# Performance work log

Measured on AMD Instinct MI355X. Metric: run time of the kernel, lower is better.

## Reference

```python
import jax, jax.numpy as jnp
import numpy as np

B = 256          # number of queries
N = 200_000      # active nodes (hidden rows / scatter dim)
E = 400_000      # edges
D = 128          # in_dim == out_dim
ATTN = 128       # attn_dim
N_REL = 24
REL_VOCAB = 2 * N_REL + 3   # 2*n_rel + 1 + 2
N_NODE = 100_000


def setup_inputs() -> dict:
    key = jax.random.key(0)
    ks = jax.random.split(key, 16)
    # forward args
    q_sub = jax.random.randint(ks[0], (B,), 0, N_NODE)
    q_rel = jax.random.randint(ks[1], (B,), 0, REL_VOCAB)
    hidden = jax.random.normal(ks[2], (N, D), dtype=jnp.float32) * 0.05
    # edges columns: [query_idx, unused, rel, tail_entity, sub_local, obj_local]
    e_q = jax.random.randint(ks[3], (E,), 0, B)
    e_unused = jnp.zeros((E,), dtype=jnp.int64)
    e_rel = jax.random.randint(ks[4], (E,), 0, REL_VOCAB)
    e_tail = jax.random.randint(ks[5], (E,), 0, N_NODE)
    e_sub = jax.random.randint(ks[6], (E,), 0, N)
    e_obj = jax.random.randint(ks[7], (E,), 0, N)
    edges = jnp.stack([e_q, e_unused, e_rel, e_tail, e_sub, e_obj], axis=1)
    nodes = jnp.stack([jax.random.randint(ks[8], (N,), 0, B),
                       jax.random.randint(ks[9], (N,), 0, N_NODE)], axis=1)
    # parameters
    rela_embed = jax.random.normal(ks[10], (REL_VOCAB, D), dtype=jnp.float32) * 0.05
    Ws = jax.random.normal(ks[11], (D, ATTN), dtype=jnp.float32) * 0.05
    Wr = jax.random.normal(ks[12], (D, ATTN), dtype=jnp.float32) * 0.05
    Wqr_w = jax.random.normal(ks[13], (D, ATTN), dtype=jnp.float32) * 0.05
    Wqr_b = jnp.zeros((ATTN,), dtype=jnp.float32)
    walpha_w = jax.random.normal(ks[14], (ATTN, 1), dtype=jnp.float32) * 0.05
    walpha_b = jnp.zeros((1,), dtype=jnp.float32)
    Wh = jax.random.normal(ks[15], (D, D), dtype=jnp.float32) * 0.05
    return {"q_sub": q_sub, "q_rel": q_rel, "hidden": hidden, "edges": edges,
            "nodes": nodes, "rela_embed": rela_embed, "Ws": Ws, "Wr": Wr,
            "Wqr_w": Wqr_w, "Wqr_b": Wqr_b, "walpha_w": walpha_w,
            "walpha_b": walpha_b, "Wh": Wh}


def reference(q_sub, q_rel, hidden, edges, nodes, rela_embed, Ws, Wr,
              Wqr_w, Wqr_b, walpha_w, walpha_b, Wh):
    # id_layer == 0 < n_layer-1: no edge filtering branch, act = identity
    sampled_nodes_idx = (nodes[:, 1] > -1) & (nodes[:, 1] < N_NODE + 1)
    sub = edges[:, 4]
    rel = edges[:, 2]
    obj = edges[:, 5]
    r_idx = edges[:, 0]
    hs = hidden[sub]                      # [E, D] gather
    hr = rela_embed[rel]                  # [E, D] gather
    h_qr = rela_embed[q_rel][r_idx]       # [B, D] -> [E, D] gather
    # fused attention MLP: sigmoid(w_alpha(relu(Ws hs + Wr hr + Wqr h_qr + b)))
    pre = jax.nn.relu(hs @ Ws + hr @ Wr + h_qr @ Wqr_w + Wqr_b)   # [E, ATTN]
    alpha = jax.nn.sigmoid(pre @ walpha_w + walpha_b)             # [E, 1]
    message = alpha * (hs + hr)                                   # [E, D]
    message_agg = jax.ops.segment_sum(message, obj, num_segments=N)  # [N, D]
    hidden_new = message_agg @ Wh                                 # [N, D]
    return hidden_new, alpha, sampled_nodes_idx
```

## Files before the change

kernel.cpp:

```cpp
#include <hip/hip_runtime.h>
#include <hip/hip_bf16.h>
#include <math.h>

#define DIM 128
#define N_NODE_C 100000

typedef __attribute__((ext_vector_type(8))) short  bf16x8;
typedef __attribute__((ext_vector_type(4))) float  f32x4;

__device__ inline unsigned short f2bf_rne(float f) {
    unsigned u = __float_as_uint(f);
    return (unsigned short)((u + 0x7FFFu + ((u >> 16) & 1u)) >> 16);
}
__device__ inline float bf2f(unsigned short u) {
    return __uint_as_float(((unsigned)u) << 16);
}

__global__ __launch_bounds__(128) void setup_kernel(
    const int* __restrict__ q_rel,
    const float* __restrict__ rela,
    const float* __restrict__ Wqr_w,
    const float* __restrict__ Wqr_b,
    const float* __restrict__ Wr,
    const float* __restrict__ Ws,
    const float* __restrict__ Wh,
    float* __restrict__ qrW,
    float* __restrict__ relhr,
    uint4* __restrict__ wpack_s,
    uint4* __restrict__ wpack_h,
    int B, int RV)
{
    const int blk = blockIdx.x;
    const int j   = threadIdx.x;

    if (blk < B + RV) {
        __shared__ float emb[DIM];
        const float* W;
        float* out;
        float bias = 0.f;
        int row;
        if (blk < B) {
            row  = q_rel[blk];
            W    = Wqr_w;
            out  = qrW + (size_t)blk * DIM;
            bias = Wqr_b[j];
        } else {
            row = blk - B;
            W   = Wr;
            out = relhr + (size_t)(blk - B) * 256;
        }
        emb[j] = rela[(size_t)row * DIM + j];
        __syncthreads();

        float acc = bias;
#pragma unroll 8
        for (int k = 0; k < DIM; ++k)
            acc += emb[k] * W[k * DIM + j];
        out[j] = acc;
        if (blk >= B)
            out[128 + j] = emb[j];
        return;
    }

    const int pid = blk - (B + RV);
    const float* W = (pid < 16) ? Ws : Wh;
    uint4* dst     = (pid < 16) ? wpack_s : wpack_h;
    const int id   = (pid & 15) * 128 + j;
    const int ct   = id >> 8;
    const int kb   = (id >> 6) & 3;
    const int lane = id & 63;
    const int col  = ct * 16 + (lane & 15);
    const int k0   = kb * 32 + (lane >> 4) * 8;

    unsigned v[4];
#pragma unroll
    for (int p = 0; p < 4; ++p) {
        unsigned lo = f2bf_rne(W[(size_t)(k0 + 2 * p)     * DIM + col]);
        unsigned hi = f2bf_rne(W[(size_t)(k0 + 2 * p + 1) * DIM + col]);
        v[p] = lo | (hi << 16);
    }
    dst[id] = make_uint4(v[0], v[1], v[2], v[3]);
}

__global__ __launch_bounds__(256) void gemm_hist_kernel(
    const float* __restrict__ A, const uint4* __restrict__ Wpack,
    unsigned short* __restrict__ H, int M,
    const int* __restrict__ edges, int* __restrict__ deg, int E, int Nb)
{
    if ((int)blockIdx.x >= Nb) {
        int i = ((int)blockIdx.x - Nb) * 256 + threadIdx.x;
        if (i < E) atomicAdd(&deg[edges[(size_t)i * 6 + 5]], 1);
        return;
    }

    __shared__ uint4 wlds[2048];
    const int t = threadIdx.x;
#pragma unroll
    for (int p = 0; p < 8; ++p)
        wlds[p * 256 + t] = Wpack[p * 256 + t];
    __syncthreads();

    const int wave = t >> 6;
    const int lane = t & 63;
    const int r    = lane & 15;
    const int g    = lane >> 4;
    const int row0 = blockIdx.x * 64 + wave * 16;

    int arow = row0 + r;
    if (arow >= M) arow = M - 1;
    const float* Ap = A + (size_t)arow * DIM + g * 8;

    bf16x8 afrag[4];
#pragma unroll
    for (int kb = 0; kb < 4; ++kb) {
        const float4 lo = *(const float4*)(Ap + kb * 32);
        const float4 hi = *(const float4*)(Ap + kb * 32 + 4);
        bf16x8 a;
        a[0] = (short)f2bf_rne(lo.x); a[1] = (short)f2bf_rne(lo.y);
        a[2] = (short)f2bf_rne(lo.z); a[3] = (short)f2bf_rne(lo.w);
        a[4] = (short)f2bf_rne(hi.x); a[5] = (short)f2bf_rne(hi.y);
        a[6] = (short)f2bf_rne(hi.z); a[7] = (short)f2bf_rne(hi.w);
        afrag[kb] = a;
    }

#pragma unroll
    for (int kb = 0; kb < 4; ++kb)
        *(bf16x8*)&H[(size_t)arow * 256 + kb * 32 + g * 8] = afrag[kb];

#pragma unroll
    for (int ct = 0; ct < 8; ++ct) {
        f32x4 acc = {0.f, 0.f, 0.f, 0.f};
#pragma unroll
        for (int kb = 0; kb < 4; ++kb) {
            bf16x8 b = *(bf16x8*)&wlds[ct * 256 + kb * 64 + lane];
            acc = __builtin_amdgcn_mfma_f32_16x16x32_bf16(afrag[kb], b, acc, 0, 0, 0);
        }
        const int col = ct * 16 + r;
#pragma unroll
        for (int jj = 0; jj < 4; ++jj) {
            const int row = row0 + g * 4 + jj;
            if (row < M)
                H[(size_t)row * 256 + 128 + col] = f2bf_rne(acc[jj]);
        }
    }
}

__global__ __launch_bounds__(256) void gemm_mfma_f32(
    const float* A, const uint4* __restrict__ Wpack, float* C, int M)
{
    __shared__ uint4 wlds[2048];
    const int t = threadIdx.x;
#pragma unroll
    for (int p = 0; p < 8; ++p)
        wlds[p * 256 + t] = Wpack[p * 256 + t];
    __syncthreads();

    const int wave = t >> 6;
    const int lane = t & 63;
    const int r    = lane & 15;
    const int g    = lane >> 4;
    const int row0 = blockIdx.x * 64 + wave * 16;

    int arow = row0 + r;
    if (arow >= M) arow = M - 1;
    const float* Ap = A + (size_t)arow * DIM + g * 8;

    bf16x8 afrag[4];
#pragma unroll
    for (int kb = 0; kb < 4; ++kb) {
        const float4 lo = *(const float4*)(Ap + kb * 32);
        const float4 hi = *(const float4*)(Ap + kb * 32 + 4);
        bf16x8 a;
        a[0] = (short)f2bf_rne(lo.x); a[1] = (short)f2bf_rne(lo.y);
        a[2] = (short)f2bf_rne(lo.z); a[3] = (short)f2bf_rne(lo.w);
        a[4] = (short)f2bf_rne(hi.x); a[5] = (short)f2bf_rne(hi.y);
        a[6] = (short)f2bf_rne(hi.z); a[7] = (short)f2bf_rne(hi.w);
        afrag[kb] = a;
    }

#pragma unroll
    for (int ct = 0; ct < 8; ++ct) {
        f32x4 acc = {0.f, 0.f, 0.f, 0.f};
#pragma unroll
        for (int kb = 0; kb < 4; ++kb) {
            bf16x8 b = *(bf16x8*)&wlds[ct * 256 + kb * 64 + lane];
            acc = __builtin_amdgcn_mfma_f32_16x16x32_bf16(afrag[kb], b, acc, 0, 0, 0);
        }
        const int col = ct * 16 + r;
#pragma unroll
        for (int jj = 0; jj < 4; ++jj) {
            const int row = row0 + g * 4 + jj;
            if (row < M)
                C[(size_t)row * DIM + col] = acc[jj];
        }
    }
}

__global__ __launch_bounds__(256) void scan1_kernel(
    const int* __restrict__ in, int* __restrict__ out,
    int* __restrict__ bsum, int n)
{
    __shared__ int ts[256];
    const int tid  = threadIdx.x;
    const int base = blockIdx.x * 2048 + tid * 8;

    int v[8];
    int run = 0;
#pragma unroll
    for (int i = 0; i < 8; ++i) {
        int x = (base + i < n) ? in[base + i] : 0;
        v[i] = run;
        run += x;
    }
    ts[tid] = run;
    __syncthreads();
    for (int off = 1; off < 256; off <<= 1) {
        int x = (tid >= off) ? ts[tid - off] : 0;
        __syncthreads();
        ts[tid] += x;
        __syncthreads();
    }
    const int excl = ts[tid] - run;
#pragma unroll
    for (int i = 0; i < 8; ++i)
        if (base + i < n) out[base + i] = v[i] + excl;
    if (tid == 255) bsum[blockIdx.x] = ts[255];
}

__global__ __launch_bounds__(256) void scan3_kernel(
    int* __restrict__ offs, int* __restrict__ cursor,
    const int* __restrict__ bsum,
    const int* __restrict__ nodes, float* __restrict__ samp, int n)
{
    __shared__ int pref;
    if (threadIdx.x == 0) {
        int run = 0;
        const int lim = blockIdx.x >> 3;
        for (int i = 0; i < lim; ++i) run += bsum[i];
        pref = run;
    }
    __syncthreads();
    int i = blockIdx.x * 256 + threadIdx.x;
    if (i < n) {
        int v = offs[i] + pref;
        offs[i]   = v;
        cursor[i] = v;
        int nv = nodes[(size_t)i * 2 + 1];
        samp[i] = (nv > -1 && nv < N_NODE_C + 1) ? 1.f : 0.f;
    }
}

__global__ __launch_bounds__(256) void scatter_kernel(
    const int* __restrict__ edges, int* __restrict__ cursor,
    int4* __restrict__ esorted, int E)
{
    int i = blockIdx.x * 256 + threadIdx.x;
    if (i < E) {
        int4 rec;
        rec.x = edges[(size_t)i * 6 + 0];
        rec.y = edges[(size_t)i * 6 + 2];
        rec.z = edges[(size_t)i * 6 + 4];
        rec.w = i;
        int obj = edges[(size_t)i * 6 + 5];
        int pos = atomicAdd(&cursor[obj], 1);
        esorted[pos] = rec;
    }
}

__global__ __launch_bounds__(256) void node_agg_kernel(
    const int4* __restrict__ esorted,
    const unsigned short* __restrict__ hsub,
    const float* __restrict__ relhr,
    const float* __restrict__ qrW,
    const float* __restrict__ walpha_w,
    const float* __restrict__ walpha_b,
    const int* __restrict__ deg,
    const int* __restrict__ offs,
    float* __restrict__ agg,
    float* __restrict__ alpha_out,
    int N)
{
    const int o = (blockIdx.x * 256 + threadIdx.x) >> 4;
    if (o >= N) return;
    const int l16 = threadIdx.x & 15;
    const int j   = l16 * 8;

    const int d = deg[o];
    const int s = offs[o];

    const float4 wwA = *(const float4*)&walpha_w[j];
    const float4 wwB = *(const float4*)&walpha_w[j + 4];
    const float  wb  = walpha_b[0];

    float4 accA = make_float4(0.f, 0.f, 0.f, 0.f);
    float4 accB = make_float4(0.f, 0.f, 0.f, 0.f);

    int4 rec = (d > 0) ? esorted[s] : make_int4(0, 0, 0, 0);
    for (int k = 0; k < d; ++k) {
        const int4 nrec = (k + 1 < d) ? esorted[s + k + 1] : rec;

        const int r_idx = rec.x;
        const int rel   = rec.y;
        const int sub   = rec.z;

        const bf16x8 hb = *(const bf16x8*)&hsub[(size_t)sub * 256 + j];
        const bf16x8 pb = *(const bf16x8*)&hsub[(size_t)sub * 256 + 128 + j];
        const float* rr = &relhr[(size_t)rel * 256];
        const float4 bA  = *(const float4*)&rr[j];
        const float4 bB  = *(const float4*)&rr[j + 4];
        const float4 rvA = *(const float4*)&rr[128 + j];
        const float4 rvB = *(const float4*)&rr[128 + j + 4];
        const float4 cA  = *(const float4*)&qrW[(size_t)r_idx * DIM + j];
        const float4 cB  = *(const float4*)&qrW[(size_t)r_idx * DIM + j + 4];

        float sdot =
            fmaxf(bf2f((unsigned short)pb[0]) + bA.x + cA.x, 0.f) * wwA.x +
            fmaxf(bf2f((unsigned short)pb[1]) + bA.y + cA.y, 0.f) * wwA.y +
            fmaxf(bf2f((unsigned short)pb[2]) + bA.z + cA.z, 0.f) * wwA.z +
            fmaxf(bf2f((unsigned short)pb[3]) + bA.w + cA.w, 0.f) * wwA.w +
            fmaxf(bf2f((unsigned short)pb[4]) + bB.x + cB.x, 0.f) * wwB.x +
            fmaxf(bf2f((unsigned short)pb[5]) + bB.y + cB.y, 0.f) * wwB.y +
            fmaxf(bf2f((unsigned short)pb[6]) + bB.z + cB.z, 0.f) * wwB.z +
            fmaxf(bf2f((unsigned short)pb[7]) + bB.w + cB.w, 0.f) * wwB.w;

#pragma unroll
        for (int off = 8; off >= 1; off >>= 1)
            sdot += __shfl_xor(sdot, off, 16);

        const float alpha =
            __builtin_amdgcn_rcpf(1.f + __expf(-(sdot + wb)));

        accA.x += alpha * (bf2f((unsigned short)hb[0]) + rvA.x);
        accA.y += alpha * (bf2f((unsigned short)hb[1]) + rvA.y);
        accA.z += alpha * (bf2f((unsigned short)hb[2]) + rvA.z);
        accA.w += alpha * (bf2f((unsigned short)hb[3]) + rvA.w);
        accB.x += alpha * (bf2f((unsigned short)hb[4]) + rvB.x);
        accB.y += alpha * (bf2f((unsigned short)hb[5]) + rvB.y);
        accB.z += alpha * (bf2f((unsigned short)hb[6]) + rvB.z);
        accB.w += alpha * (bf2f((unsigned short)hb[7]) + rvB.w);

        if (l16 == 0) alpha_out[rec.w] = alpha;
        rec = nrec;
    }

    *(float4*)&agg[(size_t)o * DIM + j]     = accA;
    *(float4*)&agg[(size_t)o * DIM + j + 4] = accB;
}

__global__ __launch_bounds__(256) void edge_kernel_fb(
    const int* __restrict__ edges,
    const float* __restrict__ hidden,
    const float* __restrict__ rela,
    const float* __restrict__ Ws,
    const float* __restrict__ qrW,
    const float* __restrict__ relhr,
    const float* __restrict__ walpha_w,
    const float* __restrict__ walpha_b,
    float* __restrict__ agg,
    float* __restrict__ alpha_out,
    int E)
{
    const int widx = threadIdx.x >> 6;
    const int lane = threadIdx.x & 63;
    const int e    = blockIdx.x * 4 + widx;
    const bool valid = (e < E);
    const int ec   = valid ? e : 0;

    const int r_idx = edges[(size_t)ec * 6 + 0];
    const int rel   = edges[(size_t)ec * 6 + 2];
    const int sub   = edges[(size_t)ec * 6 + 4];
    const int obj   = edges[(size_t)ec * 6 + 5];

    const int j = lane * 2;

    const float2 hv = *(const float2*)&hidden[(size_t)sub * DIM + j];
    const float2 rv = *(const float2*)&rela[(size_t)rel * DIM + j];

    __shared__ float hrow[4][DIM];
    *(float2*)&hrow[widx][j] = hv;
    __syncthreads();
    float p0 = 0.f, p1 = 0.f;
#pragma unroll 4
    for (int k = 0; k < DIM; ++k) {
        float hk  = hrow[widx][k];
        float2 w2 = *(const float2*)&Ws[k * DIM + j];
        p0 += hk * w2.x;
        p1 += hk * w2.y;
    }

    const float2 b2 = *(const float2*)&relhr[(size_t)rel * 256 + j];
    const float2 c2 = *(const float2*)&qrW[(size_t)r_idx * DIM + j];
    p0 = fmaxf(p0 + b2.x + c2.x, 0.f);
    p1 = fmaxf(p1 + b2.y + c2.y, 0.f);

    const float2 ww = *(const float2*)&walpha_w[j];
    float s = p0 * ww.x + p1 * ww.y;
#pragma unroll
    for (int off = 32; off >= 1; off >>= 1)
        s += __shfl_xor(s, off, 64);

    const float alpha = 1.f / (1.f + expf(-(s + walpha_b[0])));

    if (valid) {
        const float m0 = alpha * (hv.x + rv.x);
        const float m1 = alpha * (hv.y + rv.y);
        atomicAdd(&agg[(size_t)obj * DIM + j], m0);
        atomicAdd(&agg[(size_t)obj * DIM + j + 1], m1);
        if (lane == 0) alpha_out[e] = alpha;
    }
}

__global__ __launch_bounds__(256, 3) void gemm_n128(
    const float* A,
    const float* __restrict__ W,
    float* C,
    int M)
{
    __shared__ __align__(16) float Alds[64][DIM];
    __shared__ __align__(16) float Wlds[32][DIM];

    const int t    = threadIdx.x;
    const int row0 = blockIdx.x * 64;
    const int tx   = t & 31;
    const int ty   = t >> 5;

#pragma unroll
    for (int p = 0; p < 8; ++p) {
        int idx = p * 1024 + t * 4;
        int r   = idx >> 7;
        int c   = idx & 127;
        int gr  = row0 + r;
        if (gr >= M) gr = M - 1;
        *(float4*)&Alds[r][c] = *(const float4*)&A[(size_t)gr * DIM + c];
    }

    float acc[8][4] = {};

    for (int kk = 0; kk < 4; ++kk) {
        __syncthreads();
        {
            const float* Wg = W + (size_t)kk * 32 * DIM;
#pragma unroll
            for (int p = 0; p < 4; ++p) {
                int idx = p * 1024 + t * 4;
                *(float4*)&Wlds[idx >> 7][idx & 127] = *(const float4*)&Wg[idx];
            }
        }
        __syncthreads();

#pragma unroll 2
        for (int k4 = 0; k4 < 32; k4 += 4) {
            const float4 w0 = *(const float4*)&Wlds[k4 + 0][tx * 4];
            const float4 w1 = *(const float4*)&Wlds[k4 + 1][tx * 4];
            const float4 w2 = *(const float4*)&Wlds[k4 + 2][tx * 4];
            const float4 w3 = *(const float4*)&Wlds[k4 + 3][tx * 4];
#pragma unroll
            for (int i = 0; i < 8; ++i) {
                const float4 a = *(const float4*)&Alds[ty * 8 + i][kk * 32 + k4];
                acc[i][0] = fmaf(a.w, w3.x, fmaf(a.z, w2.x, fmaf(a.y, w1.x, fmaf(a.x, w0.x, acc[i][0]))));
                acc[i][1] = fmaf(a.w, w3.y, fmaf(a.z, w2.y, fmaf(a.y, w1.y, fmaf(a.x, w0.y, acc[i][1]))));
                acc[i][2] = fmaf(a.w, w3.z, fmaf(a.z, w2.z, fmaf(a.y, w1.z, fmaf(a.x, w0.z, acc[i][2]))));
                acc[i][3] = fmaf(a.w, w3.w, fmaf(a.z, w2.w, fmaf(a.y, w1.w, fmaf(a.x, w0.w, acc[i][3]))));
            }
        }
    }
    __syncthreads();

#pragma unroll
    for (int i = 0; i < 8; ++i) {
        int gr = row0 + ty * 8 + i;
        if (gr < M) {
            float4 v = make_float4(acc[i][0], acc[i][1], acc[i][2], acc[i][3]);
            *(float4*)&C[(size_t)gr * DIM + tx * 4] = v;
        }
    }
}

__global__ __launch_bounds__(256) void nodes_kernel(
    const int* __restrict__ nodes, float* __restrict__ out, int N)
{
    int i = blockIdx.x * 256 + threadIdx.x;
    if (i < N) {
        int v = nodes[(size_t)i * 2 + 1];
        out[i] = (v > -1 && v < N_NODE_C + 1) ? 1.f : 0.f;
    }
}

extern "C" void kernel_launch(void* const* d_in, const int* in_sizes, int n_in,
                              void* d_out, int out_size, void* d_ws, size_t ws_size,
                              hipStream_t stream)
{
    const int*   q_rel    = (const int*)d_in[1];
    const float* hidden   = (const float*)d_in[2];
    const int*   edges    = (const int*)d_in[3];
    const int*   nodes    = (const int*)d_in[4];
    const float* rela     = (const float*)d_in[5];
    const float* Ws       = (const float*)d_in[6];
    const float* Wr       = (const float*)d_in[7];
    const float* Wqr_w    = (const float*)d_in[8];
    const float* Wqr_b    = (const float*)d_in[9];
    const float* walpha_w = (const float*)d_in[10];
    const float* walpha_b = (const float*)d_in[11];
    const float* Wh       = (const float*)d_in[12];

    const int B  = in_sizes[1];
    const int N  = in_sizes[2] / DIM;
    const int E  = in_sizes[3] / 6;
    const int RV = in_sizes[5] / DIM;

    float* out       = (float*)d_out;
    float* agg       = out;
    float* alpha_out = out + (size_t)N * DIM;
    float* samp      = alpha_out + (size_t)E;

    char* p = (char*)d_ws;
    float* qrW   = (float*)p;     p += (size_t)B * DIM * sizeof(float);
    float* relhr = (float*)p;     p += (size_t)RV * 256 * sizeof(float);
    uint4* wpack_s = (uint4*)p;   p += 2048 * sizeof(uint4);
    uint4* wpack_h = (uint4*)p;   p += 2048 * sizeof(uint4);
    int4*  esorted = (int4*)p;    p += (size_t)E * sizeof(int4);
    unsigned short* hsub = (unsigned short*)p;
    const size_t base_bytes = (size_t)(p - (char*)d_ws);

    const size_t need_A = base_bytes
        + (size_t)N * 256 * sizeof(unsigned short)
        + ((size_t)3 * N + 128) * sizeof(int);

    setup_kernel<<<B + RV + 32, 128, 0, stream>>>(
        q_rel, rela, Wqr_w, Wqr_b, Wr, Ws, Wh,
        qrW, relhr, wpack_s, wpack_h, B, RV);

    if (ws_size >= need_A) {
        int* deg    = (int*)(hsub + (size_t)N * 256);
        int* offs   = deg + N;
        int* cursor = offs + N;
        int* bsum   = cursor + N;

        hipMemsetAsync(deg, 0, (size_t)N * sizeof(int), stream);

        const int Nb = (N + 63) / 64;
        const int Hb = (E + 255) / 256;
        gemm_hist_kernel<<<Nb + Hb, 256, 0, stream>>>(
            hidden, wpack_s, hsub, N, edges, deg, E, Nb);

        const int nb = (N + 2047) / 2048;
        scan1_kernel<<<nb, 256, 0, stream>>>(deg, offs, bsum, N);
        scan3_kernel<<<(N + 255) / 256, 256, 0, stream>>>(
            offs, cursor, bsum, nodes, samp, N);
        scatter_kernel<<<(E + 255) / 256, 256, 0, stream>>>(
            edges, cursor, esorted, E);

        node_agg_kernel<<<(N * 16 + 255) / 256, 256, 0, stream>>>(
            esorted, hsub, relhr, qrW, walpha_w, walpha_b,
            deg, offs, agg, alpha_out, N);

        gemm_mfma_f32<<<(N + 63) / 64, 256, 0, stream>>>(agg, wpack_h, out, N);
    } else {
        hipMemsetAsync(agg, 0, (size_t)N * DIM * sizeof(float), stream);
        edge_kernel_fb<<<(E + 3) / 4, 256, 0, stream>>>(
            edges, hidden, rela, Ws, qrW, relhr, walpha_w, walpha_b,
            agg, alpha_out, E);
        gemm_n128<<<(N + 63) / 64, 256, 0, stream>>>(agg, Wh, out, N);
        nodes_kernel<<<(N + 255) / 256, 256, 0, stream>>>(nodes, samp, N);
    }
}
```

Measured before the change: 228.6 us.

## Store aggregate as bf16, deepen gather prefetch, fold deg zeroing into setup

The node aggregation kernel now writes its per-node sums as bf16 into an extra workspace buffer when the workspace is large enough. The final GEMM then reads bf16 directly instead of loading fp32 and converting, which roughly halves the traffic of that intermediate. The aggregation loop also prefetches edge records two ahead and the hsub rows one ahead, to hide gather latency. The separate memset of the degree array is replaced by extra blocks in the setup kernel, saving one launch. Rounding the aggregate to bf16 before the GEMM matches the rounding the old GEMM already applied internally, and the new path only runs if the workspace has room.

Result: slower. 253.7 us (+11.0%).

```diff
diff --git a/kernel.cpp b/kernel.cpp
--- a/kernel.cpp
+++ b/kernel.cpp
@@ -28,6 +28,7 @@
     float* __restrict__ relhr,
     uint4* __restrict__ wpack_s,
     uint4* __restrict__ wpack_h,
+    int* deg, int N,
     int B, int RV)
 {
     const int blk = blockIdx.x;
@@ -62,24 +63,32 @@
         return;
     }
 
-    const int pid = blk - (B + RV);
-    const float* W = (pid < 16) ? Ws : Wh;
-    uint4* dst     = (pid < 16) ? wpack_s : wpack_h;
-    const int id   = (pid & 15) * 128 + j;
-    const int ct   = id >> 8;
-    const int kb   = (id >> 6) & 3;
-    const int lane = id & 63;
-    const int col  = ct * 16 + (lane & 15);
-    const int k0   = kb * 32 + (lane >> 4) * 8;
-
-    unsigned v[4];
-#pragma unroll
-    for (int p = 0; p < 4; ++p) {
-        unsigned lo = f2bf_rne(W[(size_t)(k0 + 2 * p)     * DIM + col]);
-        unsigned hi = f2bf_rne(W[(size_t)(k0 + 2 * p + 1) * DIM + col]);
-        v[p] = lo | (hi << 16);
-    }
-    dst[id] = make_uint4(v[0], v[1], v[2], v[3]);
+    if (blk < B + RV + 32) {
+        const int pid = blk - (B + RV);
+        const float* W = (pid < 16) ? Ws : Wh;
+        uint4* dst     = (pid < 16) ? wpack_s : wpack_h;
+        const int id   = (pid & 15) * 128 + j;
+        const int ct   = id >> 8;
+        const int kb   = (id >> 6) & 3;
+        const int lane = id & 63;
+        const int col  = ct * 16 + (lane & 15);
+        const int k0   = kb * 32 + (lane >> 4) * 8;
+
+        unsigned v[4];
+#pragma unroll
+        for (int p = 0; p < 4; ++p) {
+            unsigned lo = f2bf_rne(W[(size_t)(k0 + 2 * p)     * DIM + col]);
+            unsigned hi = f2bf_rne(W[(size_t)(k0 + 2 * p + 1) * DIM + col]);
+            v[p] = lo | (hi << 16);
+        }
+        dst[id] = make_uint4(v[0], v[1], v[2], v[3]);
+        return;
+    }
+
+    if (deg) {
+        int i = (blk - (B + RV + 32)) * 128 + j;
+        if (i < N) deg[i] = 0;
+    }
 }
 
 __global__ __launch_bounds__(256) void gemm_hist_kernel(
@@ -145,8 +154,9 @@
     }
 }
 
-__global__ __launch_bounds__(256) void gemm_mfma_f32(
-    const float* A, const uint4* __restrict__ Wpack, float* C, int M)
+template <int ABF16>
+__global__ __launch_bounds__(256) void gemm_final(
+    const void* Av, const uint4* __restrict__ Wpack, float* C, int M)
 {
     __shared__ uint4 wlds[2048];
     const int t = threadIdx.x;
@@ -163,19 +173,26 @@
 
     int arow = row0 + r;
     if (arow >= M) arow = M - 1;
-    const float* Ap = A + (size_t)arow * DIM + g * 8;
 
     bf16x8 afrag[4];
-#pragma unroll
-    for (int kb = 0; kb < 4; ++kb) {
-        const float4 lo = *(const float4*)(Ap + kb * 32);
-        const float4 hi = *(const float4*)(Ap + kb * 32 + 4);
-        bf16x8 a;
-        a[0] = (short)f2bf_rne(lo.x); a[1] = (short)f2bf_rne(lo.y);
-        a[2] = (short)f2bf_rne(lo.z); a[3] = (short)f2bf_rne(lo.w);
-        a[4] = (short)f2bf_rne(hi.x); a[5] = (short)f2bf_rne(hi.y);
-        a[6] = (short)f2bf_rne(hi.z); a[7] = (short)f2bf_rne(hi.w);
-        afrag[kb] = a;
+    if (ABF16) {
+        const unsigned short* Ab = (const unsigned short*)Av + (size_t)arow * DIM + g * 8;
+#pragma unroll
+        for (int kb = 0; kb < 4; ++kb)
+            afrag[kb] = *(const bf16x8*)(Ab + kb * 32);
+    } else {
+        const float* Ap = (const float*)Av + (size_t)arow * DIM + g * 8;
+#pragma unroll
+        for (int kb = 0; kb < 4; ++kb) {
+            const float4 lo = *(const float4*)(Ap + kb * 32);
+            const float4 hi = *(const float4*)(Ap + kb * 32 + 4);
+            bf16x8 a;
+            a[0] = (short)f2bf_rne(lo.x); a[1] = (short)f2bf_rne(lo.y);
+            a[2] = (short)f2bf_rne(lo.z); a[3] = (short)f2bf_rne(lo.w);
+            a[4] = (short)f2bf_rne(hi.x); a[5] = (short)f2bf_rne(hi.y);
+            a[6] = (short)f2bf_rne(hi.z); a[7] = (short)f2bf_rne(hi.w);
+            afrag[kb] = a;
+        }
     }
 
 #pragma unroll
@@ -267,6 +284,7 @@
     }
 }
 
+template <int AGG_BF16>
 __global__ __launch_bounds__(256) void node_agg_kernel(
     const int4* __restrict__ esorted,
     const unsigned short* __restrict__ hsub,
@@ -277,6 +295,7 @@
     const int* __restrict__ deg,
     const int* __restrict__ offs,
     float* __restrict__ agg,
+    unsigned short* __restrict__ aggb,
     float* __restrict__ alpha_out,
     int N)
 {
@@ -295,33 +314,40 @@
     float4 accA = make_float4(0.f, 0.f, 0.f, 0.f);
     float4 accB = make_float4(0.f, 0.f, 0.f, 0.f);
 
-    int4 rec = (d > 0) ? esorted[s] : make_int4(0, 0, 0, 0);
+    int4 rec0 = make_int4(0, 0, 0, 0), rec1 = rec0;
+    bf16x8 hb0 = {}, pb0 = {};
+    if (d > 0) {
+        rec0 = esorted[s];
+        hb0 = *(const bf16x8*)&hsub[(size_t)rec0.z * 256 + j];
+        pb0 = *(const bf16x8*)&hsub[(size_t)rec0.z * 256 + 128 + j];
+        rec1 = (d > 1) ? esorted[s + 1] : rec0;
+    }
+
     for (int k = 0; k < d; ++k) {
-        const int4 nrec = (k + 1 < d) ? esorted[s + k + 1] : rec;
-
-        const int r_idx = rec.x;
-        const int rel   = rec.y;
-        const int sub   = rec.z;
-
-        const bf16x8 hb = *(const bf16x8*)&hsub[(size_t)sub * 256 + j];
-        const bf16x8 pb = *(const bf16x8*)&hsub[(size_t)sub * 256 + 128 + j];
-        const float* rr = &relhr[(size_t)rel * 256];
+        const int4 rec2 = (k + 2 < d) ? esorted[s + k + 2] : rec1;
+        bf16x8 hb1 = hb0, pb1 = pb0;
+        if (k + 1 < d) {
+            hb1 = *(const bf16x8*)&hsub[(size_t)rec1.z * 256 + j];
+            pb1 = *(const bf16x8*)&hsub[(size_t)rec1.z * 256 + 128 + j];
+        }
+
+        const float* rr = &relhr[(size_t)rec0.y * 256];
         const float4 bA  = *(const float4*)&rr[j];
         const float4 bB  = *(const float4*)&rr[j + 4];
         const float4 rvA = *(const float4*)&rr[128 + j];
         const float4 rvB = *(const float4*)&rr[128 + j + 4];
-        const float4 cA  = *(const float4*)&qrW[(size_t)r_idx * DIM + j];
-        const float4 cB  = *(const float4*)&qrW[(size_t)r_idx * DIM + j + 4];
+        const float4 cA  = *(const float4*)&qrW[(size_t)rec0.x * DIM + j];
+        const float4 cB  = *(const float4*)&qrW[(size_t)rec0.x * DIM + j + 4];
 
         float sdot =
-            fmaxf(bf2f((unsigned short)pb[0]) + bA.x + cA.x, 0.f) * wwA.x +
-            fmaxf(bf2f((unsigned short)pb[1]) + bA.y + cA.y, 0.f) * wwA.y +
-            fmaxf(bf2f((unsigned short)pb[2]) + bA.z + cA.z, 0.f) * wwA.z +
-            fmaxf(bf2f((unsigned short)pb[3]) + bA.w + cA.w, 0.f) * wwA.w +
-            fmaxf(bf2f((unsigned short)pb[4]) + bB.x + cB.x, 0.f) * wwB.x +
-            fmaxf(bf2f((unsigned short)pb[5]) + bB.y + cB.y, 0.f) * wwB.y +
-            fmaxf(bf2f((unsigned short)pb[6]) + bB.z + cB.z, 0.f) * wwB.z +
-            fmaxf(bf2f((unsigned short)pb[7]) + bB.w + cB.w, 0.f) * wwB.w;
+            fmaxf(bf2f((unsigned short)pb0[0]) + bA.x + cA.x, 0.f) * wwA.x +
+            fmaxf(bf2f((unsigned short)pb0[1]) + bA.y + cA.y, 0.f) * wwA.y +
+            fmaxf(bf2f((unsigned short)pb0[2]) + bA.z + cA.z, 0.f) * wwA.z +
+            fmaxf(bf2f((unsigned short)pb0[3]) + bA.w + cA.w, 0.f) * wwA.w +
+            fmaxf(bf2f((unsigned short)pb0[4]) + bB.x + cB.x, 0.f) * wwB.x +
+            fmaxf(bf2f((unsigned short)pb0[5]) + bB.y + cB.y, 0.f) * wwB.y +
+            fmaxf(bf2f((unsigned short)pb0[6]) + bB.z + cB.z, 0.f) * wwB.z +
+            fmaxf(bf2f((unsigned short)pb0[7]) + bB.w + cB.w, 0.f) * wwB.w;
 
 #pragma unroll
         for (int off = 8; off >= 1; off >>= 1)
@@ -330,21 +356,31 @@
         const float alpha =
             __builtin_amdgcn_rcpf(1.f + __expf(-(sdot + wb)));
 
-        accA.x += alpha * (bf2f((unsigned short)hb[0]) + rvA.x);
-        accA.y += alpha * (bf2f((unsigned short)hb[1]) + rvA.y);
-        accA.z += alpha * (bf2f((unsigned short)hb[2]) + rvA.z);
-        accA.w += alpha * (bf2f((unsigned short)hb[3]) + rvA.w);
-        accB.x += alpha * (bf2f((unsigned short)hb[4]) + rvB.x);
-        accB.y += alpha * (bf2f((unsigned short)hb[5]) + rvB.y);
-        accB.z += alpha * (bf2f((unsigned short)hb[6]) + rvB.z);
-        accB.w += alpha * (bf2f((unsigned short)hb[7]) + rvB.w);
-
-        if (l16 == 0) alpha_out[rec.w] = alpha;
-        rec = nrec;
-    }
-
-    *(float4*)&agg[(size_t)o * DIM + j]     = accA;
-    *(float4*)&agg[(size_t)o * DIM + j + 4] = accB;
+        accA.x += alpha * (bf2f((unsigned short)hb0[0]) + rvA.x);
+        accA.y += alpha * (bf2f((unsigned short)hb0[1]) + rvA.y);
+        accA.z += alpha * (bf2f((unsigned short)hb0[2]) + rvA.z);
+        accA.w += alpha * (bf2f((unsigned short)hb0[3]) + rvA.w);
+        accB.x += alpha * (bf2f((unsigned short)hb0[4]) + rvB.x);
+        accB.y += alpha * (bf2f((unsigned short)hb0[5]) + rvB.y);
+        accB.z += alpha * (bf2f((unsigned short)hb0[6]) + rvB.z);
+        accB.w += alpha * (bf2f((unsigned short)hb0[7]) + rvB.w);
+
+        if (l16 == 0) alpha_out[rec0.w] = alpha;
+
+        rec0 = rec1; rec1 = rec2; hb0 = hb1; pb0 = pb1;
+    }
+
+    if (AGG_BF16) {
+        bf16x8 ob;
+        ob[0] = (short)f2bf_rne(accA.x); ob[1] = (short)f2bf_rne(accA.y);
+        ob[2] = (short)f2bf_rne(accA.z); ob[3] = (short)f2bf_rne(accA.w);
+        ob[4] = (short)f2bf_rne(accB.x); ob[5] = (short)f2bf_rne(accB.y);
+        ob[6] = (short)f2bf_rne(accB.z); ob[7] = (short)f2bf_rne(accB.w);
+        *(bf16x8*)&aggb[(size_t)o * DIM + j] = ob;
+    } else {
+        *(float4*)&agg[(size_t)o * DIM + j]     = accA;
+        *(float4*)&agg[(size_t)o * DIM + j + 4] = accB;
+    }
 }
 
 __global__ __launch_bounds__(256) void edge_kernel_fb(
@@ -520,24 +556,36 @@
     uint4* wpack_h = (uint4*)p;   p += 2048 * sizeof(uint4);
     int4*  esorted = (int4*)p;    p += (size_t)E * sizeof(int4);
     unsigned short* hsub = (unsigned short*)p;
-    const size_t base_bytes = (size_t)(p - (char*)d_ws);
-
-    const size_t need_A = base_bytes
-        + (size_t)N * 256 * sizeof(unsigned short)
-        + ((size_t)3 * N + 128) * sizeof(int);
-
-    setup_kernel<<<B + RV + 32, 128, 0, stream>>>(
+    p += (size_t)N * 256 * sizeof(unsigned short);
+    const size_t pre_int_bytes = (size_t)(p - (char*)d_ws);
+    const size_t int_bytes = ((size_t)3 * N + 128) * sizeof(int);
+
+    const size_t need_A  = pre_int_bytes + int_bytes;
+    const size_t need_Ap = need_A + (size_t)N * DIM * sizeof(unsigned short);
+
+    const bool tierA  = (ws_size >= need_A);
+    const bool tierAp = (ws_size >= need_Ap);
+
+    int* deg = nullptr;
+    int* offs = nullptr;
+    int* cursor = nullptr;
+    int* bsum = nullptr;
+    unsigned short* aggb = nullptr;
+    if (tierA) {
+        char* q = (char*)d_ws + pre_int_bytes;
+        deg    = (int*)q;
+        offs   = deg + N;
+        cursor = offs + N;
+        bsum   = cursor + N;
+        if (tierAp) aggb = (unsigned short*)(bsum + 128);
+    }
+
+    const int ZB = tierA ? (N + 127) / 128 : 0;
+    setup_kernel<<<B + RV + 32 + ZB, 128, 0, stream>>>(
         q_rel, rela, Wqr_w, Wqr_b, Wr, Ws, Wh,
-        qrW, relhr, wpack_s, wpack_h, B, RV);
-
-    if (ws_size >= need_A) {
-        int* deg    = (int*)(hsub + (size_t)N * 256);
-        int* offs   = deg + N;
-        int* cursor = offs + N;
-        int* bsum   = cursor + N;
-
-        hipMemsetAsync(deg, 0, (size_t)N * sizeof(int), stream);
-
+        qrW, relhr, wpack_s, wpack_h, deg, N, B, RV);
+
+    if (tierA) {
         const int Nb = (N + 63) / 64;
         const int Hb = (E + 255) / 256;
         gemm_hist_kernel<<<Nb + Hb, 256, 0, stream>>>(
@@ -550,11 +598,19 @@
         scatter_kernel<<<(E + 255) / 256, 256, 0, stream>>>(
             edges, cursor, esorted, E);
 
-        node_agg_kernel<<<(N * 16 + 255) / 256, 256, 0, stream>>>(
-            esorted, hsub, relhr, qrW, walpha_w, walpha_b,
-            deg, offs, agg, alpha_out, N);
-
-        gemm_mfma_f32<<<(N + 63) / 64, 256, 0, stream>>>(agg, wpack_h, out, N);
+        if (tierAp) {
+            node_agg_kernel<1><<<(N * 16 + 255) / 256, 256, 0, stream>>>(
+                esorted, hsub, relhr, qrW, walpha_w, walpha_b,
+                deg, offs, agg, aggb, alpha_out, N);
+            gemm_final<1><<<(N + 63) / 64, 256, 0, stream>>>(
+                aggb, wpack_h, out, N);
+        } else {
+            node_agg_kernel<0><<<(N * 16 + 255) / 256, 256, 0, stream>>>(
+                esorted, hsub, relhr, qrW, walpha_w, walpha_b,
+                deg, offs, agg, aggb, alpha_out, N);
+            gemm_final<0><<<(N + 63) / 64, 256, 0, stream>>>(
+                agg, wpack_h, out, N);
+        }
     } else {
         hipMemsetAsync(agg, 0, (size_t)N * DIM * sizeof(float), stream);
         edge_kernel_fb<<<(E + 3) / 4, 256, 0, stream>>>(
```
